# Performance work log

Hardware: AMD Instinct MI355X
Metric: run time of the kernel (lower is better)

## Reference

```python
import jax, jax.numpy as jnp
import numpy as np

LN_EPS = 1e-5


def setup_inputs() -> dict:
    key = jax.random.key(0)
    k1, k2, k3, k4 = jax.random.split(key, 4)
    B, S, H, NH = 32, 256, 4096, 16
    scale = (2.0 ** 0.5) * ((3.0 / H) ** 0.5)
    inp = jax.random.normal(k1, (B, S, H), dtype=jnp.float32)
    mask = jax.random.randint(k2, (B, S), 0, 2, dtype=jnp.int32)  # 1 = padded key
    weight = jnp.ones((H,), dtype=jnp.float32)
    bias = jnp.zeros((H,), dtype=jnp.float32)
    qkv = jax.random.normal(k3, (H, 3 * H), dtype=jnp.float32) * scale
    o = jax.random.normal(k4, (H, H), dtype=jnp.float32) * scale
    return {"inp": inp, "mask": mask, "weight": weight, "bias": bias,
            "qkv": qkv, "o": o, "isPre": 1}


def _layer_norm(x, weight, bias):
    mu = jnp.mean(x, axis=-1, keepdims=True)
    var = jnp.mean(jnp.square(x - mu), axis=-1, keepdims=True)
    return (x - mu) * jax.lax.rsqrt(var + LN_EPS) * weight + bias


def _mha(x, mask, weight, bias, qkv, o, isPre, head_num=16):
    B, S, H = x.shape
    D = H // head_num
    xn = _layer_norm(x, weight, bias) if isPre else x
    # fused QKV projection: [B,S,3H]
    proj = jnp.einsum('bsh,hk->bsk', xn, qkv)
    q, k, v = jnp.split(proj, 3, axis=-1)
    q = q.reshape(B, S, head_num, D)
    k = k.reshape(B, S, head_num, D)
    v = v.reshape(B, S, head_num, D)
    scores = jnp.einsum('bqnd,bknd->bnqk', q, k) / jnp.sqrt(jnp.float32(D))
    # mask[b,k]==1 -> key k is padding, exclude from softmax
    neg = jnp.finfo(scores.dtype).min
    scores = jnp.where(mask[:, None, None, :] != 0, neg, scores)
    attn = jax.nn.softmax(scores, axis=-1)
    ctx = jnp.einsum('bnqk,bknd->bqnd', attn, v).reshape(B, S, H)
    out = jnp.einsum('bsh,ho->bso', ctx, o)
    if not isPre:
        out = _layer_norm(out, weight, bias)
    return out


def reference(inp, mask, weight, bias, qkv, o, isPre):
    return _mha(inp, mask, weight, bias, qkv, o, bool(isPre))
```

## Files before the change

kernel.cpp:

```cpp
#include <hip/hip_runtime.h>
#include <stdint.h>

typedef unsigned short u16;
typedef short bf16x8 __attribute__((ext_vector_type(8)));
typedef float f32x4 __attribute__((ext_vector_type(4)));

#define MFMA16(a, b, c) __builtin_amdgcn_mfma_f32_16x16x32_bf16((a), (b), (c), 0, 0, 0)

#define GLOAD_LDS16(gp, lp)                                                        \
  __builtin_amdgcn_global_load_lds((const __attribute__((address_space(1))) void*)(gp), \
                                   (__attribute__((address_space(3))) void*)(lp), 16, 0, 0)

#define BARRIER asm volatile("s_barrier" ::: "memory")
#define WAITV(n) asm volatile("s_waitcnt vmcnt(" #n ")" ::: "memory")
#define WAITL0 asm volatile("s_waitcnt lgkmcnt(0)" ::: "memory")

__device__ __forceinline__ u16 f2bf(float x) {
  union { float f; uint32_t u; } v; v.f = x;
  uint32_t r = (v.u + 0x7FFFu + ((v.u >> 16) & 1u)) >> 16;
  return (u16)r;
}

__global__ __launch_bounds__(256) void transpose_bf16(const float* __restrict__ in,
                                                      u16* __restrict__ out, int R, int C) {
  __shared__ float tile[32][33];
  int nCt = C >> 5;
  int bid = blockIdx.x;
  int r0 = (bid / nCt) << 5, c0 = (bid % nCt) << 5;
  int t = threadIdx.x;
  int r = t >> 3, cc = (t & 7) << 2;
  float4 v = *reinterpret_cast<const float4*>(in + (size_t)(r0 + r) * C + c0 + cc);
  tile[r][cc] = v.x; tile[r][cc + 1] = v.y; tile[r][cc + 2] = v.z; tile[r][cc + 3] = v.w;
  __syncthreads();
  int c = t >> 3, rr = (t & 7) << 2;
  ushort4 u;
  u.x = f2bf(tile[rr][c]);     u.y = f2bf(tile[rr + 1][c]);
  u.z = f2bf(tile[rr + 2][c]); u.w = f2bf(tile[rr + 3][c]);
  *reinterpret_cast<ushort4*>(out + (size_t)(c0 + c) * R + r0 + rr) = u;
}

__global__ __launch_bounds__(256) void ln_bf16(const float* __restrict__ in,
                                               const float* __restrict__ w,
                                               const float* __restrict__ bia,
                                               u16* __restrict__ out) {
  int row = blockIdx.x, t = threadIdx.x;
  const float* x = in + (size_t)row * 4096;
  float4 v[4];
  float s = 0.f, sq = 0.f;
#pragma unroll
  for (int i = 0; i < 4; i++) {
    v[i] = *reinterpret_cast<const float4*>(x + i * 1024 + t * 4);
    s  += v[i].x + v[i].y + v[i].z + v[i].w;
    sq += v[i].x * v[i].x + v[i].y * v[i].y + v[i].z * v[i].z + v[i].w * v[i].w;
  }
#pragma unroll
  for (int off = 32; off > 0; off >>= 1) { s += __shfl_down(s, off); sq += __shfl_down(sq, off); }
  __shared__ float red[8];
  int wid = t >> 6, lane = t & 63;
  if (lane == 0) { red[wid] = s; red[4 + wid] = sq; }
  __syncthreads();
  if (t == 0) {
    float st = red[0] + red[1] + red[2] + red[3];
    float sqt = red[4] + red[5] + red[6] + red[7];
    float mu = st * (1.f / 4096.f);
    float var = sqt * (1.f / 4096.f) - mu * mu;
    red[0] = mu; red[1] = rsqrtf(var + 1e-5f);
  }
  __syncthreads();
  float mu = red[0], rs = red[1];
#pragma unroll
  for (int i = 0; i < 4; i++) {
    float4 wv = *reinterpret_cast<const float4*>(w + i * 1024 + t * 4);
    float4 bv = *reinterpret_cast<const float4*>(bia + i * 1024 + t * 4);
    ushort4 u;
    u.x = f2bf((v[i].x - mu) * rs * wv.x + bv.x);
    u.y = f2bf((v[i].y - mu) * rs * wv.y + bv.y);
    u.z = f2bf((v[i].z - mu) * rs * wv.z + bv.z);
    u.w = f2bf((v[i].w - mu) * rs * wv.w + bv.w);
    *reinterpret_cast<ushort4*>(out + (size_t)row * 4096 + i * 1024 + t * 4) = u;
  }
}


#define LDA8(AR, Ab, mh) do {                                                     \
  _Pragma("unroll")                                                               \
  for (int mf = 0; mf < 4; mf++) {                                                \
    int lr = (mh)*128 + wm64 + mf*16 + llo;                                       \
    const char* rb = (Ab) + lr*128;                                               \
    int sw = (lr & 7) << 4;                                                       \
    AR[mf*2+0] = *reinterpret_cast<const bf16x8*>(rb + ((lhi16) ^ sw));           \
    AR[mf*2+1] = *reinterpret_cast<const bf16x8*>(rb + ((64 + lhi16) ^ sw));      \
  }                                                                               \
} while (0)

#define LDB4(BR, Bb, nh) do {                                                     \
  _Pragma("unroll")                                                               \
  for (int nf = 0; nf < 2; nf++) {                                                \
    int lr = (nh)*128 + wn32 + nf*16 + llo;                                       \
    const char* rb = (Bb) + lr*128;                                               \
    int sw = (lr & 7) << 4;                                                       \
    BR[nf*2+0] = *reinterpret_cast<const bf16x8*>(rb + ((lhi16) ^ sw));           \
    BR[nf*2+1] = *reinterpret_cast<const bf16x8*>(rb + ((64 + lhi16) ^ sw));      \
  }                                                                               \
} while (0)

#define MMAQ(AR, BR, mh, nh) do {                                                 \
  _Pragma("unroll")                                                               \
  for (int mf = 0; mf < 4; mf++)                                                  \
    _Pragma("unroll")                                                             \
    for (int nf = 0; nf < 2; nf++) {                                              \
      acc[(mh)*4+mf][(nh)*2+nf] = MFMA16(AR[mf*2+0], BR[nf*2+0], acc[(mh)*4+mf][(nh)*2+nf]); \
      acc[(mh)*4+mf][(nh)*2+nf] = MFMA16(AR[mf*2+1], BR[nf*2+1], acc[(mh)*4+mf][(nh)*2+nf]); \
    }                                                                             \
} while (0)

#define STAGE(isB, h, cbuf, ktile) do {                                           \
  const u16* g_ = (isB) ? Bt : A;                                                 \
  int base0_ = (isB) ? n0 : m0;                                                   \
  char* lb_ = smc + (cbuf)*65536 + (isB)*32768 + (h)*16384;                       \
  _Pragma("unroll")                                                               \
  for (int i_ = 0; i_ < 2; i_++) {                                                \
    int L_ = i_*512 + t;                                                          \
    int lr_ = (h)*128 + (L_ >> 3);                                                \
    int sl_ = (L_ & 7) ^ (lr_ & 7);                                               \
    int r_ = (isB) ? (((lr_ & 128) >> 2) | ((lr_ & 96) << 1) | (lr_ & 31))        \
                   : ((lr_ & 63) | ((lr_ & 64) << 1) | ((lr_ & 128) >> 1));       \
    GLOAD_LDS16(g_ + (size_t)(base0_ + r_) * K + (ktile)*64 + sl_*8, lb_ + L_*16);\
  }                                                                               \
} while (0)

#define TILE2(tt, S1, S2, W2) do {                                                \
  int c_ = (tt) & 1;                                                              \
  const char* Ab = smc + c_ * 65536;                                              \
  const char* Bb = Ab + 32768;                                                    \
          \
  LDA8(aR, Ab, 0); LDB4(b0R, Bb, 0); LDB4(b1R, Bb, 1);                            \
  if (S1) { STAGE(1, 0, c_ ^ 1, (tt) + 1); STAGE(0, 1, c_ ^ 1, (tt) + 1); }       \
  __builtin_amdgcn_s_setprio(1);                                                  \
  MMAQ(aR, b0R, 0, 0); MMAQ(aR, b1R, 0, 1);                                       \
  __builtin_amdgcn_s_setprio(0);                                                  \
  WAITL0; BARRIER;                                                                \
                                     \
  LDA8(aR, Ab, 1);                                                                \
  if (S2) { STAGE(0, 0, c_, (tt) + 2); STAGE(1, 1, c_, (tt) + 2); }               \
  __builtin_amdgcn_s_setprio(1);                                                  \
  MMAQ(aR, b1R, 1, 1); MMAQ(aR, b0R, 1, 0);                                       \
  __builtin_amdgcn_s_setprio(0);                                                  \
  WAITV(W2); WAITL0; BARRIER;                                                     \
} while (0)

template <int EPI>
__global__ __launch_bounds__(512, 2) void gemm256(const u16* __restrict__ A, const u16* __restrict__ Bt,
                                                  void* __restrict__ Cout, u16* __restrict__ vT,
                                                  int M, int N, int K, int nbn) {
  __shared__ u16 sm[65536];
  char* smc = (char*)sm;
  int bid = blockIdx.x;
  int s = bid >> 8, local = bid & 255;
  int xcd = local & 7, j = local >> 3;
  int trow = ((xcd >> 1) << 2) + (j >> 3);
  int tcol = ((xcd & 1) << 3) + (j & 7);
  int nsc = nbn >> 4;
  int sr = s / nsc, sc = s - sr * nsc;
  int tm = (sr << 4) + trow, tn = (sc << 4) + tcol;
  int m0 = tm << 8, n0 = tn << 8;
  int t = threadIdx.x;
  int w = t >> 6, lane = t & 63;
  int wm = w >> 2, wn = w & 3;
  int llo = lane & 15, lhi = lane >> 4;
  int wm64 = wm << 6, wn32 = wn << 5, lhi16 = lhi << 4;
  f32x4 acc[8][4] = {};
  bf16x8 aR[8], b0R[4], b1R[4];
  int NT = K >> 6;
  STAGE(0, 0, 0, 0); STAGE(1, 0, 0, 0); STAGE(1, 1, 0, 0); STAGE(0, 1, 0, 0);
  STAGE(0, 0, 1, 1); STAGE(1, 1, 1, 1);
  WAITV(4); BARRIER;
#pragma unroll 1
  for (int tt = 0; tt < NT - 2; ++tt) TILE2(tt, 1, 1, 4);
  TILE2(NT - 2, 1, 0, 0);
  TILE2(NT - 1, 0, 0, 0);
  if (EPI == 2) {
    float* C = (float*)Cout;
#pragma unroll
    for (int mi = 0; mi < 8; mi++)
#pragma unroll
      for (int ni = 0; ni < 4; ni++) {
        int m = m0 + wm * 128 + mi * 16 + lhi * 4;
        int n = n0 + wn * 64 + ni * 16 + llo;
#pragma unroll
        for (int r = 0; r < 4; r++) C[(size_t)(m + r) * N + n] = acc[mi][ni][r];
      }
  } else {
    if (n0 < 8192) {
      u16* qkb = (u16*)Cout;
#pragma unroll
      for (int mi = 0; mi < 8; mi++)
#pragma unroll
        for (int ni = 0; ni < 4; ni++) {
          int m = m0 + wm * 128 + mi * 16 + lhi * 4;
          int n = n0 + wn * 64 + ni * 16 + llo;
#pragma unroll
          for (int r = 0; r < 4; r++) qkb[(size_t)(m + r) * 8192 + n] = f2bf(acc[mi][ni][r]);
        }
    } else {
#pragma unroll
      for (int mi = 0; mi < 8; mi++)
#pragma unroll
        for (int ni = 0; ni < 4; ni++) {
          int m = m0 + wm * 128 + mi * 16 + lhi * 4;
          int n_ = n0 + wn * 64 + ni * 16 + llo - 8192;
          int h = n_ >> 8, d = n_ & 255;
          int b = m >> 8, s2 = m & 255;
          ushort4 u;
          u.x = f2bf(acc[mi][ni][0]); u.y = f2bf(acc[mi][ni][1]);
          u.z = f2bf(acc[mi][ni][2]); u.w = f2bf(acc[mi][ni][3]);
          *reinterpret_cast<ushort4*>(vT + ((size_t)((b << 4) + h) * 256 + d) * 256 + s2) = u;
        }
    }
  }
}

__global__ __launch_bounds__(256) void attn_kernel(const u16* __restrict__ qk,
                                                   const u16* __restrict__ vT,
                                                   const int* __restrict__ mask,
                                                   u16* __restrict__ ctx) {
  __shared__ u16 KV[64 * 256];
  __shared__ u16 P[64 * 256];
  __shared__ float maskf[256];
  int bx = blockIdx.x;
  int qt = bx & 3, h = (bx >> 2) & 15, b = bx >> 6;
  int t = threadIdx.x, wid = t >> 6, lane = t & 63, llo = lane & 15, lhi = lane >> 4;
  maskf[t] = mask[(b << 8) + t] ? -1e30f : 0.0f;
  bf16x8 qf[8];
  {
    const u16* qrow = qk + (size_t)((b << 8) + (qt << 6) + (wid << 4) + llo) * 8192 + (h << 8);
#pragma unroll
    for (int c = 0; c < 8; c++)
      qf[c] = *reinterpret_cast<const bf16x8*>(qrow + (lhi << 3) + (c << 5));
  }
  f32x4 sacc[16] = {};
#pragma unroll 1
  for (int kt = 0; kt < 4; kt++) {
    __syncthreads();
#pragma unroll
    for (int i = 0; i < 8; i++) {
      int G = (i << 8) + t;
      int key = G >> 5, g = G & 31;
      int gs = g ^ (key & 7);
      const u16* src = qk + (size_t)((b << 8) + (kt << 6) + key) * 8192 + 4096 + (h << 8) + (gs << 3);
      GLOAD_LDS16(src, (char*)KV + (G << 4));
    }
    __syncthreads();
#pragma unroll
    for (int nf = 0; nf < 4; nf++) {
      int kl = (nf << 4) + llo;
      const char* kb = (const char*)KV + (kl << 9);
      int sw = (kl & 7) << 4;
#pragma unroll
      for (int c = 0; c < 8; c++) {
        bf16x8 kf = *reinterpret_cast<const bf16x8*>(kb + (((lhi << 4) + (c << 6)) ^ sw));
        sacc[kt * 4 + nf] = MFMA16(qf[c], kf, sacc[kt * 4 + nf]);
      }
    }
  }
  float madd[16];
#pragma unroll
  for (int f = 0; f < 16; f++)
    madd[f] = maskf[((f >> 2) << 6) + ((f & 3) << 4) + llo];
  float mx[4] = {-3e38f, -3e38f, -3e38f, -3e38f};
#pragma unroll
  for (int f = 0; f < 16; f++)
#pragma unroll
    for (int r = 0; r < 4; r++) {
      float sv = sacc[f][r] * 0.0625f + madd[f];
      sacc[f][r] = sv;
      mx[r] = fmaxf(mx[r], sv);
    }
#pragma unroll
  for (int r = 0; r < 4; r++)
#pragma unroll
    for (int d = 1; d < 16; d <<= 1) mx[r] = fmaxf(mx[r], __shfl_xor(mx[r], d));
  float sum[4] = {0.f, 0.f, 0.f, 0.f};
#pragma unroll
  for (int f = 0; f < 16; f++)
#pragma unroll
    for (int r = 0; r < 4; r++) {
      float p = __expf(sacc[f][r] - mx[r]);
      sacc[f][r] = p;
      sum[r] += p;
    }
#pragma unroll
  for (int r = 0; r < 4; r++)
#pragma unroll
    for (int d = 1; d < 16; d <<= 1) sum[r] += __shfl_xor(sum[r], d);
  float rin[4];
#pragma unroll
  for (int r = 0; r < 4; r++) rin[r] = 1.f / sum[r];
#pragma unroll
  for (int r = 0; r < 4; r++) {
    int q = (wid << 4) + (lhi << 2) + r;
    char* pb = (char*)P + (q << 9);
    int sw = (q & 7) << 4;
#pragma unroll
    for (int f = 0; f < 16; f++) {
      int key = ((f >> 2) << 6) + ((f & 3) << 4) + llo;
      *reinterpret_cast<u16*>(pb + ((key << 1) ^ sw)) = f2bf(sacc[f][r] * rin[r]);
    }
  }
  f32x4 cacc[16] = {};
#pragma unroll 1
  for (int kt = 0; kt < 4; kt++) {
    __syncthreads();
#pragma unroll
    for (int i = 0; i < 8; i++) {
      int G = (i << 8) + t;
      int d = G >> 3, g = G & 7;
      int gs = g ^ (d & 7);
      const u16* src = vT + ((size_t)((b << 4) + h) * 256 + d) * 256 + (kt << 6) + (gs << 3);
      GLOAD_LDS16(src, (char*)KV + (G << 4));
    }
    __syncthreads();
    bf16x8 pf[2];
    {
      int q = (wid << 4) + llo;
      const char* pb = (const char*)P + (q << 9);
      int sw = (q & 7) << 4;
#pragma unroll
      for (int c = 0; c < 2; c++)
        pf[c] = *reinterpret_cast<const bf16x8*>(pb + (((kt << 7) + (c << 6) + (lhi << 4)) ^ sw));
    }
#pragma unroll
    for (int mf = 0; mf < 16; mf++) {
      int dl = (mf << 4) + llo;
      const char* vb = (const char*)KV + (dl << 7);
      int sw = (dl & 7) << 4;
#pragma unroll
      for (int c = 0; c < 2; c++) {
        bf16x8 vf = *reinterpret_cast<const bf16x8*>(vb + (((lhi << 4) + (c << 6)) ^ sw));
        cacc[mf] = MFMA16(vf, pf[c], cacc[mf]);
      }
    }
  }
  int token = (b << 8) + (qt << 6) + (wid << 4) + llo;
  u16* crow = ctx + (size_t)token * 4096 + (h << 8);
#pragma unroll
  for (int mf = 0; mf < 16; mf++) {
    ushort4 u;
    u.x = f2bf(cacc[mf][0]); u.y = f2bf(cacc[mf][1]);
    u.z = f2bf(cacc[mf][2]); u.w = f2bf(cacc[mf][3]);
    *reinterpret_cast<ushort4*>(crow + (mf << 4) + (lhi << 2)) = u;
  }
}

extern "C" void kernel_launch(void* const* d_in, const int* in_sizes, int n_in,
                              void* d_out, int out_size, void* d_ws, size_t ws_size,
                              hipStream_t stream) {
  const float* inp  = (const float*)d_in[0];
  const int*   mask = (const int*)d_in[1];
  const float* w    = (const float*)d_in[2];
  const float* bia  = (const float*)d_in[3];
  const float* qkvw = (const float*)d_in[4];
  const float* ow   = (const float*)d_in[5];
  const size_t MB = 1024ull * 1024ull;
  if (ws_size < 352 * MB) return;
  char* ws = (char*)d_ws;
  u16* xn   = (u16*)(ws);
  u16* qkvT = (u16*)(ws + 64 * MB);
  u16* qk   = (u16*)(ws + 160 * MB);
  u16* vT   = (u16*)(ws + 288 * MB);
  u16* oT   = (u16*)(ws + 64 * MB);
  u16* ctx  = (u16*)(ws);
  float* out = (float*)d_out;

  transpose_bf16<<<49152, 256, 0, stream>>>(qkvw, qkvT, 4096, 12288);
  ln_bf16<<<8192, 256, 0, stream>>>(inp, w, bia, xn);
  gemm256<1><<<1536, 512, 0, stream>>>(xn, qkvT, (void*)qk, vT, 8192, 12288, 4096, 48);
  transpose_bf16<<<16384, 256, 0, stream>>>(ow, oT, 4096, 4096);
  attn_kernel<<<2048, 256, 0, stream>>>(qk, vT, mask, ctx);
  gemm256<2><<<512, 512, 0, stream>>>(ctx, oT, (void*)out, nullptr, 8192, 4096, 4096, 16);
}
```

Baseline: 1.265 ms.

## Load K/V fragments directly from global, remap attention blocks per XCD, widen transpose tiles

The attention kernel stops staging K and V tiles through LDS with barriers. Each lane now reads its MFMA fragments straight from global memory, and the mask is read directly instead of through a shared array. Blocks are remapped so the four query tiles of a (batch, head) pair land on the same XCD, which is meant to raise L2 reuse of K and V. The weight transpose kernel now uses 64x64 tiles with 16-byte bf16 stores and a quarter of the blocks. The trade-off is redundant, less coalesced global reads per wave in exchange for removing the LDS copies and barriers.

```diff
diff --git a/kernel.cpp b/kernel.cpp
--- a/kernel.cpp
+++ b/kernel.cpp
@@ -4,6 +4,7 @@
 typedef unsigned short u16;
 typedef short bf16x8 __attribute__((ext_vector_type(8)));
 typedef float f32x4 __attribute__((ext_vector_type(4)));
+typedef unsigned short u16x8 __attribute__((ext_vector_type(8)));
 
 #define MFMA16(a, b, c) __builtin_amdgcn_mfma_f32_16x16x32_bf16((a), (b), (c), 0, 0, 0)
 
@@ -23,20 +24,29 @@
 
 __global__ __launch_bounds__(256) void transpose_bf16(const float* __restrict__ in,
                                                       u16* __restrict__ out, int R, int C) {
-  __shared__ float tile[32][33];
-  int nCt = C >> 5;
+  __shared__ float tile[64][65];
+  int nCt = C >> 6;
   int bid = blockIdx.x;
-  int r0 = (bid / nCt) << 5, c0 = (bid % nCt) << 5;
+  int r0 = (bid / nCt) << 6, c0 = (bid % nCt) << 6;
   int t = threadIdx.x;
-  int r = t >> 3, cc = (t & 7) << 2;
-  float4 v = *reinterpret_cast<const float4*>(in + (size_t)(r0 + r) * C + c0 + cc);
-  tile[r][cc] = v.x; tile[r][cc + 1] = v.y; tile[r][cc + 2] = v.z; tile[r][cc + 3] = v.w;
+  int r = t >> 2, cg = (t & 3) << 4;
+  const float* src = in + (size_t)(r0 + r) * C + c0 + cg;
+#pragma unroll
+  for (int i = 0; i < 4; i++) {
+    float4 v = *reinterpret_cast<const float4*>(src + (i << 2));
+    tile[r][cg + (i << 2) + 0] = v.x; tile[r][cg + (i << 2) + 1] = v.y;
+    tile[r][cg + (i << 2) + 2] = v.z; tile[r][cg + (i << 2) + 3] = v.w;
+  }
   __syncthreads();
-  int c = t >> 3, rr = (t & 7) << 2;
-  ushort4 u;
-  u.x = f2bf(tile[rr][c]);     u.y = f2bf(tile[rr + 1][c]);
-  u.z = f2bf(tile[rr + 2][c]); u.w = f2bf(tile[rr + 3][c]);
-  *reinterpret_cast<ushort4*>(out + (size_t)(c0 + c) * R + r0 + rr) = u;
+  int c = t >> 2, rg = (t & 3) << 4;
+  u16* dst = out + (size_t)(c0 + c) * R + r0 + rg;
+#pragma unroll
+  for (int i = 0; i < 2; i++) {
+    u16x8 o8;
+#pragma unroll
+    for (int j2 = 0; j2 < 8; j2++) o8[j2] = f2bf(tile[rg + (i << 3) + j2][c]);
+    *reinterpret_cast<u16x8*>(dst + (i << 3)) = o8;
+  }
 }
 
 __global__ __launch_bounds__(256) void ln_bf16(const float* __restrict__ in,
@@ -224,13 +234,13 @@
                                                    const u16* __restrict__ vT,
                                                    const int* __restrict__ mask,
                                                    u16* __restrict__ ctx) {
-  __shared__ u16 KV[64 * 256];
   __shared__ u16 P[64 * 256];
-  __shared__ float maskf[256];
-  int bx = blockIdx.x;
-  int qt = bx & 3, h = (bx >> 2) & 15, b = bx >> 6;
+  int bid = blockIdx.x;
+  int xcd = bid & 7, idx = bid >> 3;
+  int qt = idx & 3;
+  int bh = (xcd << 6) + (idx >> 2);
+  int b = bh >> 4, h = bh & 15;
   int t = threadIdx.x, wid = t >> 6, lane = t & 63, llo = lane & 15, lhi = lane >> 4;
-  maskf[t] = mask[(b << 8) + t] ? -1e30f : 0.0f;
   bf16x8 qf[8];
   {
     const u16* qrow = qk + (size_t)((b << 8) + (qt << 6) + (wid << 4) + llo) * 8192 + (h << 8);
@@ -239,34 +249,25 @@
       qf[c] = *reinterpret_cast<const bf16x8*>(qrow + (lhi << 3) + (c << 5));
   }
   f32x4 sacc[16] = {};
+  const u16* kbase = qk + (size_t)(b << 8) * 8192 + 4096 + (h << 8) + (lhi << 3);
 #pragma unroll 1
   for (int kt = 0; kt < 4; kt++) {
-    __syncthreads();
-#pragma unroll
-    for (int i = 0; i < 8; i++) {
-      int G = (i << 8) + t;
-      int key = G >> 5, g = G & 31;
-      int gs = g ^ (key & 7);
-      const u16* src = qk + (size_t)((b << 8) + (kt << 6) + key) * 8192 + 4096 + (h << 8) + (gs << 3);
-      GLOAD_LDS16(src, (char*)KV + (G << 4));
-    }
-    __syncthreads();
 #pragma unroll
     for (int nf = 0; nf < 4; nf++) {
-      int kl = (nf << 4) + llo;
-      const char* kb = (const char*)KV + (kl << 9);
-      int sw = (kl & 7) << 4;
+      const u16* krow = kbase + (size_t)((kt << 6) + (nf << 4) + llo) * 8192;
 #pragma unroll
       for (int c = 0; c < 8; c++) {
-        bf16x8 kf = *reinterpret_cast<const bf16x8*>(kb + (((lhi << 4) + (c << 6)) ^ sw));
+        bf16x8 kf = *reinterpret_cast<const bf16x8*>(krow + (c << 5));
         sacc[kt * 4 + nf] = MFMA16(qf[c], kf, sacc[kt * 4 + nf]);
       }
     }
   }
   float madd[16];
 #pragma unroll
-  for (int f = 0; f < 16; f++)
-    madd[f] = maskf[((f >> 2) << 6) + ((f & 3) << 4) + llo];
+  for (int f = 0; f < 16; f++) {
+    int key = ((f >> 2) << 6) + ((f & 3) << 4) + llo;
+    madd[f] = mask[(b << 8) + key] ? -1e30f : 0.0f;
+  }
   float mx[4] = {-3e38f, -3e38f, -3e38f, -3e38f};
 #pragma unroll
   for (int f = 0; f < 16; f++)
@@ -307,19 +308,11 @@
       *reinterpret_cast<u16*>(pb + ((key << 1) ^ sw)) = f2bf(sacc[f][r] * rin[r]);
     }
   }
+  WAITL0;
   f32x4 cacc[16] = {};
+  const u16* vbase = vT + (size_t)bh * 65536 + (lhi << 3);
 #pragma unroll 1
   for (int kt = 0; kt < 4; kt++) {
-    __syncthreads();
-#pragma unroll
-    for (int i = 0; i < 8; i++) {
-      int G = (i << 8) + t;
-      int d = G >> 3, g = G & 7;
-      int gs = g ^ (d & 7);
-      const u16* src = vT + ((size_t)((b << 4) + h) * 256 + d) * 256 + (kt << 6) + (gs << 3);
-      GLOAD_LDS16(src, (char*)KV + (G << 4));
-    }
-    __syncthreads();
     bf16x8 pf[2];
     {
       int q = (wid << 4) + llo;
@@ -331,12 +324,10 @@
     }
 #pragma unroll
     for (int mf = 0; mf < 16; mf++) {
-      int dl = (mf << 4) + llo;
-      const char* vb = (const char*)KV + (dl << 7);
-      int sw = (dl & 7) << 4;
+      const u16* vrow = vbase + (size_t)((mf << 4) + llo) * 256 + (kt << 6);
 #pragma unroll
       for (int c = 0; c < 2; c++) {
-        bf16x8 vf = *reinterpret_cast<const bf16x8*>(vb + (((lhi << 4) + (c << 6)) ^ sw));
+        bf16x8 vf = *reinterpret_cast<const bf16x8*>(vrow + (c << 5));
         cacc[mf] = MFMA16(vf, pf[c], cacc[mf]);
       }
     }
@@ -372,10 +363,10 @@
   u16* ctx  = (u16*)(ws);
   float* out = (float*)d_out;
 
-  transpose_bf16<<<49152, 256, 0, stream>>>(qkvw, qkvT, 4096, 12288);
+  transpose_bf16<<<12288, 256, 0, stream>>>(qkvw, qkvT, 4096, 12288);
   ln_bf16<<<8192, 256, 0, stream>>>(inp, w, bia, xn);
   gemm256<1><<<1536, 512, 0, stream>>>(xn, qkvT, (void*)qk, vT, 8192, 12288, 4096, 48);
-  transpose_bf16<<<16384, 256, 0, stream>>>(ow, oT, 4096, 4096);
+  transpose_bf16<<<4096, 256, 0, stream>>>(ow, oT, 4096, 4096);
   attn_kernel<<<2048, 256, 0, stream>>>(qk, vT, mask, ctx);
   gemm256<2><<<512, 512, 0, stream>>>(ctx, oT, (void*)out, nullptr, 8192, 4096, 4096, 16);
 }
```

Result: slower. 1.424 ms (+12.6%).
